# Optimization experiments

Measured on AMD Instinct MI355X. Metric: run time of the kernel, lower is better.

Reference implementation:

```python
import jax, jax.numpy as jnp
import numpy as np

C, U, V, D, B = 5, 6144, 6144, 64, 4096  # classes, users, items, feat dim, batch pairs


def setup_inputs() -> dict:
    key = jax.random.key(0)
    ks = jax.random.split(key, 16)
    s = 1.0 / np.sqrt(D)
    adj = (jax.random.uniform(ks[0], (C, U, V)) < 0.01).astype(jnp.float32)
    return {
        "u": jax.random.randint(ks[1], (B,), 0, U),
        "v": jax.random.randint(ks[2], (B,), 0, V),
        "u_emb": jax.random.normal(ks[3], (U, D), jnp.float32) * 0.1,
        "v_emb": jax.random.normal(ks[4], (V, D), jnp.float32) * 0.1,
        "W1u": jax.random.normal(ks[5], (C, D, D), jnp.float32) * s,
        "b1u": jnp.zeros((C, D), jnp.float32),
        "W1v": jax.random.normal(ks[6], (C, D, D), jnp.float32) * s,
        "b1v": jnp.zeros((C, D), jnp.float32),
        "W2u": jax.random.normal(ks[7], (C, D, D), jnp.float32) * s,
        "b2u": jnp.zeros((C, D), jnp.float32),
        "W2v": jax.random.normal(ks[8], (C, D, D), jnp.float32) * s,
        "b2v": jnp.zeros((C, D), jnp.float32),
        "Q": jax.random.normal(ks[9], (C, D, D), jnp.float32) * s,
        "adj": adj,
    }


def reference(u, v, u_emb, v_emb, W1u, b1u, W1v, b1v, W2u, b2u, W2v, b2v, Q, adj):
    # ---- layer 1: per-class graph convolution, summed over rating classes ----
    # user codes aggregate item features through adj_c; item codes through adj_c^T
    msg_v = jnp.einsum("vd,cde->cve", v_emb, W1v)            # [C,V,D]
    h_u = jax.nn.relu(jnp.einsum("cuv,cve->ue", adj, msg_v) + b1v.sum(0))  # [U,D]
    msg_u = jnp.einsum("ud,cde->cue", u_emb, W1u)            # [C,U,D]
    h_v = jax.nn.relu(jnp.einsum("cuv,cue->ve", adj, msg_u) + b1u.sum(0))  # [V,D]
    # ---- layer 2 ----
    z_u = jnp.einsum("cuv,cve->ue", adj, jnp.einsum("vd,cde->cve", h_v, W2u)) + b2u.sum(0)
    z_v = jnp.einsum("cuv,cue->ve", adj, jnp.einsum("ud,cde->cue", h_u, W2v)) + b2v.sum(0)
    # ---- bilinear decoder over batch of (user, item) pairs ----
    zu = z_u[u]                                              # [B,D] gather
    zv = z_v[v]                                              # [B,D] gather
    logits = jnp.einsum("bd,cde,be->bc", zu, Q, zv)          # [B,C] per-class rating logits
    return logits
```

## Files before the change

### kernel.cpp

```cpp
#include <hip/hip_runtime.h>

#define NC   5
#define NU   6144
#define NV   6144
#define ND   64
#define NB   4096
#define CAP  128
#define HALF (NC * NU)

__device__ __forceinline__ unsigned int spread4(unsigned int x) {
  x &= 0xFFu;
  x = (x | (x << 12)) & 0x000F000Fu;
  x = (x | (x << 6))  & 0x03030303u;
  x = (x | (x << 3))  & 0x11111111u;
  return x;
}

__global__ __launch_bounds__(256) void k_adj2idx(
    const float* __restrict__ adj,
    int* __restrict__ cnt,
    unsigned short* __restrict__ idx) {
  __shared__ unsigned int rowwords[64][9];
  const int b = blockIdx.x;
  const int c  = b / 2304;
  const int rem = b - c * 2304;
  const int tu = rem / 24;
  const int tv = rem - tu * 24;
  const int wave = threadIdx.x >> 6;
  const int lane = threadIdx.x & 63;

  float4 av[16];
  {
    const float* base = adj +
        ((size_t)(c * NU + tu * 64 + wave * 16) * NV + tv * 256);
    #pragma unroll
    for (int rr = 0; rr < 16; ++rr)
      av[rr] = ((const float4*)(base + (size_t)rr * NV))[lane];
  }
  #pragma unroll
  for (int rr = 0; rr < 16; ++rr) {
    const unsigned long long b0 = __ballot(av[rr].x != 0.0f);
    const unsigned long long b1 = __ballot(av[rr].y != 0.0f);
    const unsigned long long b2 = __ballot(av[rr].z != 0.0f);
    const unsigned long long b3 = __ballot(av[rr].w != 0.0f);
    if (lane < 8) {
      const unsigned int e0 = spread4((unsigned int)(b0 >> (lane * 8)));
      const unsigned int e1 = spread4((unsigned int)(b1 >> (lane * 8)));
      const unsigned int e2 = spread4((unsigned int)(b2 >> (lane * 8)));
      const unsigned int e3 = spread4((unsigned int)(b3 >> (lane * 8)));
      rowwords[wave * 16 + rr][lane] = e0 | (e1 << 1) | (e2 << 2) | (e3 << 3);
    }
  }
  __syncthreads();

  #pragma unroll
  for (int p = 0; p < 2; ++p) {
    const int rloc = lane >> 3;
    const int wloc = lane & 7;
    const int r = wave * 16 + p * 8 + rloc;
    const unsigned int wbits = rowwords[r][wloc];
    const int pc = __popc(wbits);
    int pre = pc;
    #pragma unroll
    for (int d = 1; d < 8; d <<= 1) {
      const int y = __shfl_up(pre, d, 64);
      if (wloc >= d) pre += y;
    }
    const int total = __shfl(pre, rloc * 8 + 7, 64);
    const int excl  = pre - pc;
    const int R = c * 6144 + tu * 64 + r;
    int base = 0;
    if (wloc == 0 && total > 0) base = atomicAdd(&cnt[R], total);
    base = __shfl(base, rloc * 8, 64);
    unsigned int m = wbits;
    int o = base + excl;
    unsigned short* orow = idx + (size_t)R * CAP;
    const int vbase = tv * 256 + wloc * 32;
    while (m) {
      const int bb = __ffs(m) - 1;
      if (o < CAP) orow[o] = (unsigned short)(vbase + bb);
      ++o;
      m &= m - 1;
    }
  }

  {
    const int j = threadIdx.x;
    const int w = j >> 5, bit = j & 31;
    unsigned int w0 = 0, w1 = 0;
    #pragma unroll
    for (int r = 0; r < 32; ++r) {
      w0 |= ((rowwords[r][w]      >> bit) & 1u) << r;
      w1 |= ((rowwords[r + 32][w] >> bit) & 1u) << r;
    }
    const int cj = __popc(w0) + __popc(w1);
    if (cj > 0) {
      const int R = (NC + c) * 6144 + tv * 256 + j;
      int o = atomicAdd(&cnt[R], cj);
      unsigned short* orow = idx + (size_t)R * CAP;
      const int ubase = tu * 64;
      unsigned int m = w0;
      while (m) {
        const int bb = __ffs(m) - 1;
        if (o < CAP) orow[o] = (unsigned short)(ubase + bb);
        ++o;
        m &= m - 1;
      }
      m = w1;
      while (m) {
        const int bb = __ffs(m) - 1;
        if (o < CAP) orow[o] = (unsigned short)(ubase + 32 + bb);
        ++o;
        m &= m - 1;
      }
    }
  }
}

__global__ __launch_bounds__(256) void k_gather(
    const int* __restrict__ cnt,
    const unsigned short* __restrict__ idx,
    const float* __restrict__ tabA,
    const float* __restrict__ tabB,
    float* __restrict__ agg) {
  __shared__ float4 red4[4][16];
  const int wave = threadIdx.x >> 6;
  const int lane = threadIdx.x & 63;
  const int R = blockIdx.x * 4 + wave;
  const int g    = lane >> 4;
  const int e16  = lane & 15;
  int n = cnt[R];
  n = n > CAP ? CAP : n;
  const unsigned short* l = idx + (size_t)R * CAP;
  const float4* tab = (const float4*)(R < HALF ? tabA : tabB);
  float4 a0 = make_float4(0.f,0.f,0.f,0.f), a1 = a0, a2 = a0, a3 = a0;
  int i = 0;
  for (; i + 16 <= n; i += 16) {
    const int j0 = l[i + g], j1 = l[i + 4 + g];
    const int j2 = l[i + 8 + g], j3 = l[i + 12 + g];
    const float4 x0 = tab[j0 * 16 + e16];
    const float4 x1 = tab[j1 * 16 + e16];
    const float4 x2 = tab[j2 * 16 + e16];
    const float4 x3 = tab[j3 * 16 + e16];
    a0.x += x0.x; a0.y += x0.y; a0.z += x0.z; a0.w += x0.w;
    a1.x += x1.x; a1.y += x1.y; a1.z += x1.z; a1.w += x1.w;
    a2.x += x2.x; a2.y += x2.y; a2.z += x2.z; a2.w += x2.w;
    a3.x += x3.x; a3.y += x3.y; a3.z += x3.z; a3.w += x3.w;
  }
  for (; i + 4 <= n; i += 4) {
    const float4 x = tab[(int)l[i + g] * 16 + e16];
    a0.x += x.x; a0.y += x.y; a0.z += x.z; a0.w += x.w;
  }
  if (i + g < n) {
    const float4 x = tab[(int)l[i + g] * 16 + e16];
    a1.x += x.x; a1.y += x.y; a1.z += x.z; a1.w += x.w;
  }
  a0.x += a1.x + a2.x + a3.x;
  a0.y += a1.y + a2.y + a3.y;
  a0.z += a1.z + a2.z + a3.z;
  a0.w += a1.w + a2.w + a3.w;
  #pragma unroll
  for (int off = 16; off < 64; off <<= 1) {
    a0.x += __shfl_xor(a0.x, off, 64);
    a0.y += __shfl_xor(a0.y, off, 64);
    a0.z += __shfl_xor(a0.z, off, 64);
    a0.w += __shfl_xor(a0.w, off, 64);
  }
  if (g == 0) red4[wave][e16] = a0;
  __syncthreads();
  if (g == 0) ((float4*)agg)[(size_t)R * 16 + e16] = red4[wave][e16];
}

__global__ __launch_bounds__(256) void k_gemm5(
    const float* __restrict__ agg,
    const float* __restrict__ Wa, const float* __restrict__ ba,
    float* __restrict__ outA,
    const float* __restrict__ Wb, const float* __restrict__ bb,
    float* __restrict__ outB,
    int do_relu) {
  const int half = blockIdx.x >= 384;
  const float* W    = half ? Wb : Wa;
  const float* bias = half ? bb : ba;
  float* out        = half ? outB : outA;
  const float* aggh = agg + (size_t)half * HALF * 64;
  const int lane = threadIdx.x & 63;
  const int wave = threadIdx.x >> 6;
  const int r0 = (blockIdx.x - half * 384) * 16 + wave * 4;
  float bs = 0.0f;
  #pragma unroll
  for (int c = 0; c < NC; ++c) bs += bias[c * 64 + lane];
  float acc[4] = {bs, bs, bs, bs};
  for (int c = 0; c < NC; ++c) {
    float w[64];
    #pragma unroll
    for (int d = 0; d < 64; ++d) w[d] = W[c * 4096 + d * 64 + lane];
    #pragma unroll
    for (int r = 0; r < 4; ++r) {
      const float4* ar = (const float4*)(aggh + ((size_t)c * 6144 + r0 + r) * 64);
      #pragma unroll
      for (int d4 = 0; d4 < 16; ++d4) {
        const float4 a = ar[d4];
        acc[r] = fmaf(a.x, w[d4 * 4 + 0], acc[r]);
        acc[r] = fmaf(a.y, w[d4 * 4 + 1], acc[r]);
        acc[r] = fmaf(a.z, w[d4 * 4 + 2], acc[r]);
        acc[r] = fmaf(a.w, w[d4 * 4 + 3], acc[r]);
      }
    }
  }
  #pragma unroll
  for (int r = 0; r < 4; ++r) {
    const float x = do_relu ? fmaxf(acc[r], 0.0f) : acc[r];
    out[(size_t)(r0 + r) * 64 + lane] = x;
  }
}

__global__ __launch_bounds__(256) void k_decoder(
    const int* __restrict__ uu, const int* __restrict__ vv,
    const float* __restrict__ z_u, const float* __restrict__ z_v,
    const float* __restrict__ Q,
    float* __restrict__ out) {
  const int lane = threadIdx.x & 63;
  const int wave = threadIdx.x >> 6;
  const int b = blockIdx.x * 4 + wave;
  const int ub = uu[b];
  const int vb = vv[b];
  const float zve = z_v[(size_t)vb * 64 + lane];
  const float* zu = z_u + (size_t)ub * 64;
  #pragma unroll
  for (int c = 0; c < NC; ++c) {
    const float* Qc = Q + c * 64 * 64;
    float t = 0.0f;
    #pragma unroll
    for (int d = 0; d < 64; ++d) t = fmaf(zu[d], Qc[d * 64 + lane], t);
    float p = t * zve;
    #pragma unroll
    for (int off = 32; off > 0; off >>= 1) p += __shfl_xor(p, off, 64);
    if (lane == 0) out[(size_t)b * NC + c] = p;
  }
}

extern "C" void kernel_launch(void* const* d_in, const int* in_sizes, int n_in,
                              void* d_out, int out_size, void* d_ws, size_t ws_size,
                              hipStream_t stream) {
  const int*   u     = (const int*)d_in[0];
  const int*   v     = (const int*)d_in[1];
  const float* u_emb = (const float*)d_in[2];
  const float* v_emb = (const float*)d_in[3];
  const float* W1u   = (const float*)d_in[4];
  const float* b1u   = (const float*)d_in[5];
  const float* W1v   = (const float*)d_in[6];
  const float* b1v   = (const float*)d_in[7];
  const float* W2u   = (const float*)d_in[8];
  const float* b2u   = (const float*)d_in[9];
  const float* W2v   = (const float*)d_in[10];
  const float* b2v   = (const float*)d_in[11];
  const float* Q     = (const float*)d_in[12];
  const float* adj   = (const float*)d_in[13];
  float* out = (float*)d_out;

  char* ws = (char*)d_ws;
  int* cnt = (int*)ws;
  unsigned short* idxL = (unsigned short*)(ws + 245760);
  char* fbase = ws + 245760 + 15728640;
  float* agg = (float*)fbase;
  float* h_u = (float*)(fbase + 15728640);
  float* h_v = (float*)(fbase + 17301504);
  float* z_u = (float*)(fbase + 18874368);
  float* z_v = (float*)(fbase + 20447232);

  hipMemsetAsync(cnt, 0, 2 * NC * 6144 * sizeof(int), stream);

  k_adj2idx<<<NC * 96 * 24, 256, 0, stream>>>(adj, cnt, idxL);

  k_gather<<<2 * HALF / 4, 256, 0, stream>>>(cnt, idxL, v_emb, u_emb, agg);
  k_gemm5<<<768, 256, 0, stream>>>(agg, W1v, b1v, h_u, W1u, b1u, h_v, 1);
  k_gather<<<2 * HALF / 4, 256, 0, stream>>>(cnt, idxL, h_v, h_u, agg);
  k_gemm5<<<768, 256, 0, stream>>>(agg, W2u, b2u, z_u, W2v, b2v, z_v, 0);
  k_decoder<<<NB / 4, 256, 0, stream>>>(u, v, z_u, z_v, Q, out);
}
```

Measured before the change: 1.171 ms.

## Fuse neighbor gather into per-class GEMM via LDS and remap adjacency block order

The separate gather and GEMM kernels are merged into one layer kernel. Each block gathers its 16 rows for all 5 classes into shared memory and then applies the weight transform directly, so the 15 MB agg buffer is no longer written and re-read through global memory. The adj2idx block index is also remapped so that groups of 8 consecutive blocks cover different row tiles at the same column tile, which changes the DRAM access pattern. The fused kernel launches only 768 blocks that each do serial gathers (20 rows per wave), so it trades the old kernel's 15360-block latency hiding for lower occupancy and less parallelism.

```diff
diff --git a/kernel.cpp b/kernel.cpp
--- a/kernel.cpp
+++ b/kernel.cpp
@@ -21,11 +21,12 @@
     int* __restrict__ cnt,
     unsigned short* __restrict__ idx) {
   __shared__ unsigned int rowwords[64][9];
-  const int b = blockIdx.x;
-  const int c  = b / 2304;
-  const int rem = b - c * 2304;
-  const int tu = rem / 24;
-  const int tv = rem - tu * 24;
+  const int x = blockIdx.x & 7;
+  const int s = blockIdx.x >> 3;
+  const int tv = s % 24;
+  const int S = (s / 24) * 8 + x;
+  const int c  = S / 96;
+  const int tu = S - c * 96;
   const int wave = threadIdx.x >> 6;
   const int lane = threadIdx.x & 63;
 
@@ -117,75 +118,72 @@
   }
 }
 
-__global__ __launch_bounds__(256) void k_gather(
+__global__ __launch_bounds__(256) void k_layer(
     const int* __restrict__ cnt,
     const unsigned short* __restrict__ idx,
     const float* __restrict__ tabA,
     const float* __restrict__ tabB,
-    float* __restrict__ agg) {
-  __shared__ float4 red4[4][16];
-  const int wave = threadIdx.x >> 6;
-  const int lane = threadIdx.x & 63;
-  const int R = blockIdx.x * 4 + wave;
-  const int g    = lane >> 4;
-  const int e16  = lane & 15;
-  int n = cnt[R];
-  n = n > CAP ? CAP : n;
-  const unsigned short* l = idx + (size_t)R * CAP;
-  const float4* tab = (const float4*)(R < HALF ? tabA : tabB);
-  float4 a0 = make_float4(0.f,0.f,0.f,0.f), a1 = a0, a2 = a0, a3 = a0;
-  int i = 0;
-  for (; i + 16 <= n; i += 16) {
-    const int j0 = l[i + g], j1 = l[i + 4 + g];
-    const int j2 = l[i + 8 + g], j3 = l[i + 12 + g];
-    const float4 x0 = tab[j0 * 16 + e16];
-    const float4 x1 = tab[j1 * 16 + e16];
-    const float4 x2 = tab[j2 * 16 + e16];
-    const float4 x3 = tab[j3 * 16 + e16];
-    a0.x += x0.x; a0.y += x0.y; a0.z += x0.z; a0.w += x0.w;
-    a1.x += x1.x; a1.y += x1.y; a1.z += x1.z; a1.w += x1.w;
-    a2.x += x2.x; a2.y += x2.y; a2.z += x2.z; a2.w += x2.w;
-    a3.x += x3.x; a3.y += x3.y; a3.z += x3.z; a3.w += x3.w;
-  }
-  for (; i + 4 <= n; i += 4) {
-    const float4 x = tab[(int)l[i + g] * 16 + e16];
-    a0.x += x.x; a0.y += x.y; a0.z += x.z; a0.w += x.w;
-  }
-  if (i + g < n) {
-    const float4 x = tab[(int)l[i + g] * 16 + e16];
-    a1.x += x.x; a1.y += x.y; a1.z += x.z; a1.w += x.w;
-  }
-  a0.x += a1.x + a2.x + a3.x;
-  a0.y += a1.y + a2.y + a3.y;
-  a0.z += a1.z + a2.z + a3.z;
-  a0.w += a1.w + a2.w + a3.w;
-  #pragma unroll
-  for (int off = 16; off < 64; off <<= 1) {
-    a0.x += __shfl_xor(a0.x, off, 64);
-    a0.y += __shfl_xor(a0.y, off, 64);
-    a0.z += __shfl_xor(a0.z, off, 64);
-    a0.w += __shfl_xor(a0.w, off, 64);
-  }
-  if (g == 0) red4[wave][e16] = a0;
-  __syncthreads();
-  if (g == 0) ((float4*)agg)[(size_t)R * 16 + e16] = red4[wave][e16];
-}
-
-__global__ __launch_bounds__(256) void k_gemm5(
-    const float* __restrict__ agg,
     const float* __restrict__ Wa, const float* __restrict__ ba,
     float* __restrict__ outA,
     const float* __restrict__ Wb, const float* __restrict__ bb,
     float* __restrict__ outB,
     int do_relu) {
-  const int half = blockIdx.x >= 384;
-  const float* W    = half ? Wb : Wa;
-  const float* bias = half ? bb : ba;
-  float* out        = half ? outB : outA;
-  const float* aggh = agg + (size_t)half * HALF * 64;
+  __shared__ float4 lds_agg[NC][16][16];
+  const int side = blockIdx.x >= 384;
+  const int r0   = (blockIdx.x - side * 384) * 16;
+  const float4* tab = (const float4*)(side ? tabB : tabA);
+  const float* W    = side ? Wb : Wa;
+  const float* bias = side ? bb : ba;
+  float* out        = side ? outB : outA;
+  const int wave = threadIdx.x >> 6;
   const int lane = threadIdx.x & 63;
-  const int wave = threadIdx.x >> 6;
-  const int r0 = (blockIdx.x - half * 384) * 16 + wave * 4;
+  const int g    = lane >> 4;
+  const int e16  = lane & 15;
+
+  for (int rr = wave * 4; rr < wave * 4 + 4; ++rr) {
+    for (int c = 0; c < NC; ++c) {
+      const int R = side * HALF + c * 6144 + r0 + rr;
+      int n = cnt[R];
+      n = n > CAP ? CAP : n;
+      const unsigned short* l = idx + (size_t)R * CAP;
+      float4 a0 = make_float4(0.f,0.f,0.f,0.f), a1 = a0, a2 = a0, a3 = a0;
+      int i = 0;
+      for (; i + 16 <= n; i += 16) {
+        const int j0 = l[i + g], j1 = l[i + 4 + g];
+        const int j2 = l[i + 8 + g], j3 = l[i + 12 + g];
+        const float4 x0 = tab[j0 * 16 + e16];
+        const float4 x1 = tab[j1 * 16 + e16];
+        const float4 x2 = tab[j2 * 16 + e16];
+        const float4 x3 = tab[j3 * 16 + e16];
+        a0.x += x0.x; a0.y += x0.y; a0.z += x0.z; a0.w += x0.w;
+        a1.x += x1.x; a1.y += x1.y; a1.z += x1.z; a1.w += x1.w;
+        a2.x += x2.x; a2.y += x2.y; a2.z += x2.z; a2.w += x2.w;
+        a3.x += x3.x; a3.y += x3.y; a3.z += x3.z; a3.w += x3.w;
+      }
+      for (; i + 4 <= n; i += 4) {
+        const float4 x = tab[(int)l[i + g] * 16 + e16];
+        a0.x += x.x; a0.y += x.y; a0.z += x.z; a0.w += x.w;
+      }
+      if (i + g < n) {
+        const float4 x = tab[(int)l[i + g] * 16 + e16];
+        a1.x += x.x; a1.y += x.y; a1.z += x.z; a1.w += x.w;
+      }
+      a0.x += a1.x + a2.x + a3.x;
+      a0.y += a1.y + a2.y + a3.y;
+      a0.z += a1.z + a2.z + a3.z;
+      a0.w += a1.w + a2.w + a3.w;
+      #pragma unroll
+      for (int off = 16; off < 64; off <<= 1) {
+        a0.x += __shfl_xor(a0.x, off, 64);
+        a0.y += __shfl_xor(a0.y, off, 64);
+        a0.z += __shfl_xor(a0.z, off, 64);
+        a0.w += __shfl_xor(a0.w, off, 64);
+      }
+      if (g == 0) lds_agg[c][rr][e16] = a0;
+    }
+  }
+  __syncthreads();
+
   float bs = 0.0f;
   #pragma unroll
   for (int c = 0; c < NC; ++c) bs += bias[c * 64 + lane];
@@ -196,10 +194,9 @@
     for (int d = 0; d < 64; ++d) w[d] = W[c * 4096 + d * 64 + lane];
     #pragma unroll
     for (int r = 0; r < 4; ++r) {
-      const float4* ar = (const float4*)(aggh + ((size_t)c * 6144 + r0 + r) * 64);
       #pragma unroll
       for (int d4 = 0; d4 < 16; ++d4) {
-        const float4 a = ar[d4];
+        const float4 a = lds_agg[c][wave * 4 + r][d4];
         acc[r] = fmaf(a.x, w[d4 * 4 + 0], acc[r]);
         acc[r] = fmaf(a.y, w[d4 * 4 + 1], acc[r]);
         acc[r] = fmaf(a.z, w[d4 * 4 + 2], acc[r]);
@@ -209,8 +206,8 @@
   }
   #pragma unroll
   for (int r = 0; r < 4; ++r) {
-    const float x = do_relu ? fmaxf(acc[r], 0.0f) : acc[r];
-    out[(size_t)(r0 + r) * 64 + lane] = x;
+    const float v = do_relu ? fmaxf(acc[r], 0.0f) : acc[r];
+    out[(size_t)(r0 + wave * 4 + r) * 64 + lane] = v;
   }
 }
 
@@ -262,19 +259,18 @@
   int* cnt = (int*)ws;
   unsigned short* idxL = (unsigned short*)(ws + 245760);
   char* fbase = ws + 245760 + 15728640;
-  float* agg = (float*)fbase;
-  float* h_u = (float*)(fbase + 15728640);
-  float* h_v = (float*)(fbase + 17301504);
-  float* z_u = (float*)(fbase + 18874368);
-  float* z_v = (float*)(fbase + 20447232);
+  float* h_u = (float*)fbase;
+  float* h_v = (float*)(fbase + 1572864);
+  float* z_u = (float*)(fbase + 3145728);
+  float* z_v = (float*)(fbase + 4718592);
 
   hipMemsetAsync(cnt, 0, 2 * NC * 6144 * sizeof(int), stream);
 
   k_adj2idx<<<NC * 96 * 24, 256, 0, stream>>>(adj, cnt, idxL);
 
-  k_gather<<<2 * HALF / 4, 256, 0, stream>>>(cnt, idxL, v_emb, u_emb, agg);
-  k_gemm5<<<768, 256, 0, stream>>>(agg, W1v, b1v, h_u, W1u, b1u, h_v, 1);
-  k_gather<<<2 * HALF / 4, 256, 0, stream>>>(cnt, idxL, h_v, h_u, agg);
-  k_gemm5<<<768, 256, 0, stream>>>(agg, W2u, b2u, z_u, W2v, b2v, z_v, 0);
+  k_layer<<<768, 256, 0, stream>>>(cnt, idxL, v_emb, u_emb,
+                                   W1v, b1v, h_u, W1u, b1u, h_v, 1);
+  k_layer<<<768, 256, 0, stream>>>(cnt, idxL, h_v, h_u,
+                                   W2u, b2u, z_u, W2v, b2v, z_v, 0);
   k_decoder<<<NB / 4, 256, 0, stream>>>(u, v, z_u, z_v, Q, out);
 }
```

Measured after the change: 1.165 ms. Within noise of the previous version (-0.6%).
